# Optimization experiments

Hardware: AMD Instinct MI355X
Metric: run time of the kernel (lower is better)

## Reference

```python
import jax, jax.numpy as jnp
import numpy as np
from jax.scipy.special import erf

ALPHA = 0.84
SSIM_WIN = 11       # monai SSIMLoss default win_size
SIGMA = 1.5         # both kernels use sigma=1.5
K1, K2, DATA_RANGE = 0.01, 0.03, 1.0


def _erf_gauss_1d(sigma=SIGMA, truncated=4.0):
    # monai.networks.layers.gaussian_1d, approx='erf', normalize=False
    tail = int(max(sigma * truncated, 0.5) + 0.5)  # 6 -> 13 taps
    x = jnp.arange(-tail, tail + 1, dtype=jnp.float32)
    t = 0.70710678 / sigma
    out = 0.5 * (erf(t * (x + 0.5)) - erf(t * (x - 0.5)))
    return jnp.clip(out, 0.0)


def _ssim_gauss_1d(win=SSIM_WIN, sigma=SIGMA):
    # monai SSIM gaussian kernel: exp-based, normalized
    d = jnp.arange(-(win - 1) / 2.0, (win + 1) / 2.0, dtype=jnp.float32)
    g = jnp.exp(-(d ** 2) / (2.0 * sigma ** 2))
    return g / g.sum()


def _conv1d(x, k, axis, pad):
    # depthwise 1D conv along spatial axis of NCHW tensor (C=1)
    ks = k.shape[0]
    if axis == 2:
        kern = k.reshape(1, 1, ks, 1)
        p = [(pad, pad), (0, 0)]
    else:
        kern = k.reshape(1, 1, 1, ks)
        p = [(0, 0), (pad, pad)]
    return jax.lax.conv_general_dilated(
        x, kern, window_strides=(1, 1), padding=p,
        dimension_numbers=('NCHW', 'OIHW', 'NCHW'))


def _sep_filter(x, k, pad):
    return _conv1d(_conv1d(x, k, 2, pad), k, 3, pad)


def setup_inputs() -> dict:
    key = jax.random.key(0)
    kx, ky = jax.random.split(key)
    shape = (64, 1, 512, 512)
    x = jax.random.uniform(kx, shape, dtype=jnp.float32)
    y = jax.random.uniform(ky, shape, dtype=jnp.float32)
    return {"x": x, "y": y}


def reference(x, y):
    kw = _ssim_gauss_1d()
    filt = lambda t: _sep_filter(t, kw, 0)
    c1 = (K1 * DATA_RANGE) ** 2
    c2 = (K2 * DATA_RANGE) ** 2
    mx, my = filt(x), filt(y)
    mxx, myy, mxy = filt(x * x), filt(y * y), filt(x * y)
    vx = mxx - mx * mx
    vy = myy - my * my
    cov = mxy - mx * my
    ssim = ((2.0 * mx * my + c1) * (2.0 * cov + c2)) / (
        (mx * mx + my * my + c1) * (vx + vy + c2))
    ssim_loss = 1.0 - jnp.mean(ssim)  # scalar, reduction='mean'

    # --- L1 branch: SAME zero-padded erf-gaussian filtering, no reduction ---
    ke = _erf_gauss_1d()
    pad = (ke.shape[0] - 1) // 2
    l1 = jnp.abs(_sep_filter(y, ke, pad) - _sep_filter(x, ke, pad))  # [N,1,H,W]

    return 100.0 * (ALPHA * ssim_loss + (1.0 - ALPHA) * l1)
```

## Files before the change

### kernel.cpp

```cpp
#include <hip/hip_runtime.h>
#include <cmath>

#define IMG_W 512
#define IMG_H 512
#define NIMG 64
#define OWV 502

struct KTaps {
    float kw[11];
    float ke[13];
};

__global__ __launch_bounds__(256) void ssim_band_kernel(
        const float* __restrict__ x, const float* __restrict__ y,
        double* __restrict__ ssum, KTaps kt) {
    __shared__ __align__(16) float sx[2][272];
    __shared__ __align__(16) float sy[2][272];

    const int img   = blockIdx.z;
    const int band  = blockIdx.y;
    const int strip = blockIdx.x;
    const int tid   = threadIdx.x;
    const int r0    = band * 64;
    const int c0    = strip * 256;

    const float* __restrict__ xi = x + (size_t)img * IMG_H * IMG_W;
    const float* __restrict__ yi = y + (size_t)img * IMG_H * IMG_W;

    float w12[12];
#pragma unroll
    for (int j = 0; j < 12; ++j) w12[j] = 0.f;
    if (tid & 1) {
#pragma unroll
        for (int j = 0; j < 11; ++j) w12[j + 1] = kt.kw[j];
    } else {
#pragma unroll
        for (int j = 0; j < 11; ++j) w12[j] = kt.kw[j];
    }

    float acc[11][5];
#pragma unroll
    for (int i = 0; i < 11; ++i)
#pragma unroll
        for (int q = 0; q < 5; ++q) acc[i][q] = 0.f;
    float tsum = 0.f;

    const int basei = tid & ~1;
    const int outc  = c0 + tid;

    auto ldx = [&](int r, int g) -> float2 {
        float2 v = make_float2(0.f, 0.f);
        if (r < IMG_H && g < IMG_W) v = *(const float2*)(xi + (size_t)r * IMG_W + g);
        return v;
    };
    auto ldy = [&](int r, int g) -> float2 {
        float2 v = make_float2(0.f, 0.f);
        if (r < IMG_H && g < IMG_W) v = *(const float2*)(yi + (size_t)r * IMG_W + g);
        return v;
    };

    if (tid < 133) { float2 v = ldx(r0, c0 + 2 * tid); *(float2*)&sx[0][2 * tid] = v; }
    if (tid >= 123) { const int t3 = tid - 123; float2 v = ldy(r0, c0 + 2 * t3); *(float2*)&sy[0][2 * t3] = v; }
    __syncthreads();

#pragma unroll 1
    for (int chunk = 0; chunk < 7; ++chunk) {
#pragma unroll
        for (int p = 0; p < 11; ++p) {
            const int rr = chunk * 11 + p;
            if (rr <= 73) {
                const int b = rr & 1;
                float2 px = make_float2(0.f, 0.f), py = make_float2(0.f, 0.f);
                const bool pre = (rr < 73);
                if (pre) {
                    if (tid < 133) px = ldx(r0 + rr + 1, c0 + 2 * tid);
                    if (tid >= 123) py = ldy(r0 + rr + 1, c0 + 2 * (tid - 123));
                }
                float xv[12], yv[12];
#pragma unroll
                for (int j = 0; j < 6; ++j) {
                    const float2 a = *(const float2*)&sx[b][basei + 2 * j];
                    const float2 c = *(const float2*)&sy[b][basei + 2 * j];
                    xv[2 * j] = a.x; xv[2 * j + 1] = a.y;
                    yv[2 * j] = c.x; yv[2 * j + 1] = c.y;
                }
                float h0 = 0.f, h1 = 0.f, h2 = 0.f, h3 = 0.f, h4 = 0.f;
#pragma unroll
                for (int j = 0; j < 12; ++j) {
                    const float w = w12[j];
                    const float a = xv[j], bb = yv[j];
                    h0 += w * a;
                    h1 += w * bb;
                    h2 += w * (a * a);
                    h3 += w * (bb * bb);
                    h4 += w * (a * bb);
                }
#pragma unroll
                for (int d = 0; d <= 10; ++d) {
                    const int s = (p + 11 - d) % 11;
                    const float w = kt.kw[d];
                    acc[s][0] += w * h0; acc[s][1] += w * h1; acc[s][2] += w * h2;
                    acc[s][3] += w * h3; acc[s][4] += w * h4;
                }
                {
                    const int sc = (p + 1) % 11;
                    const int ro = rr - 10;
                    if (ro >= 0) {
                        const int o = r0 + ro;
                        if (o < OWV && outc < OWV) {
                            const float mx = acc[sc][0], my = acc[sc][1];
                            const float vx = acc[sc][2] - mx * mx;
                            const float vy = acc[sc][3] - my * my;
                            const float cov = acc[sc][4] - mx * my;
                            const float c1 = 1e-4f, c2 = 9e-4f;
                            tsum += ((2.f * mx * my + c1) * (2.f * cov + c2)) /
                                    ((mx * mx + my * my + c1) * (vx + vy + c2));
                        }
                    }
#pragma unroll
                    for (int q = 0; q < 5; ++q) acc[sc][q] = 0.f;
                }
                if (pre) {
                    const int bn = b ^ 1;
                    if (tid < 133) *(float2*)&sx[bn][2 * tid] = px;
                    if (tid >= 123) *(float2*)&sy[bn][2 * (tid - 123)] = py;
                }
                __syncthreads();
            }
        }
    }

#pragma unroll
    for (int off = 32; off > 0; off >>= 1) tsum += __shfl_down(tsum, off, 64);
    __shared__ float wsum[4];
    const int wid = tid >> 6, lane = tid & 63;
    if (lane == 0) wsum[wid] = tsum;
    __syncthreads();
    if (tid == 0) atomicAdd(ssum, (double)(wsum[0] + wsum[1] + wsum[2] + wsum[3]));
}

__global__ __launch_bounds__(256) void l1_band_kernel(
        const float* __restrict__ x, const float* __restrict__ y,
        const double* __restrict__ ssum, float* __restrict__ out, KTaps kt) {
    __shared__ __align__(16) float sd[2][528];

    const int img  = blockIdx.y;
    const int band = blockIdx.x;
    const int tid  = threadIdx.x;
    const int o0   = band * 32;
    const int rin0 = o0 - 6;

    const float* __restrict__ xi = x + (size_t)img * IMG_H * IMG_W;
    const float* __restrict__ yi = y + (size_t)img * IMG_H * IMG_W;
    float* __restrict__ oi = out + (size_t)img * IMG_H * IMG_W;

    const float base = 100.f * 0.84f * (1.f - (float)(*ssum) * (1.f / 16128256.f));

    float acc[13][2];
#pragma unroll
    for (int i = 0; i < 13; ++i) { acc[i][0] = 0.f; acc[i][1] = 0.f; }

    if (tid < 12) {
        const int idx = (tid < 6) ? tid : (512 + tid);
        sd[0][idx] = 0.f; sd[1][idx] = 0.f;
    }

    auto ldd = [&](int r) -> float2 {
        float2 v = make_float2(0.f, 0.f);
        if (r >= 0 && r < IMG_H) {
            const float2 a = *(const float2*)(xi + (size_t)r * IMG_W + 2 * tid);
            const float2 bb = *(const float2*)(yi + (size_t)r * IMG_W + 2 * tid);
            v = make_float2(bb.x - a.x, bb.y - a.y);
        }
        return v;
    };

    { float2 v = ldd(rin0); *(float2*)&sd[0][6 + 2 * tid] = v; }
    __syncthreads();

#pragma unroll 1
    for (int chunk = 0; chunk < 4; ++chunk) {
#pragma unroll
        for (int p = 0; p < 13; ++p) {
            const int rr = chunk * 13 + p;
            if (rr <= 43) {
                const int b = rr & 1;
                float2 pv = make_float2(0.f, 0.f);
                const bool pre = (rr < 43);
                if (pre) pv = ldd(rin0 + rr + 1);

                float dv[14];
#pragma unroll
                for (int j = 0; j < 7; ++j) {
                    const float2 a = *(const float2*)&sd[b][2 * tid + 2 * j];
                    dv[2 * j] = a.x; dv[2 * j + 1] = a.y;
                }
                float a0 = 0.f, a1 = 0.f;
#pragma unroll
                for (int u = 0; u < 13; ++u) {
                    a0 += kt.ke[u] * dv[u];
                    a1 += kt.ke[u] * dv[u + 1];
                }
#pragma unroll
                for (int dd = 0; dd <= 12; ++dd) {
                    const int s = (p + 13 - dd) % 13;
                    acc[s][0] += kt.ke[dd] * a0;
                    acc[s][1] += kt.ke[dd] * a1;
                }
                {
                    const int sc = (p + 1) % 13;
                    const int ro = rr - 12;
                    if (ro >= 0) {
                        const int o = o0 + ro;
                        *(float2*)&oi[(size_t)o * IMG_W + 2 * tid] =
                            make_float2(base + 16.f * fabsf(acc[sc][0]),
                                        base + 16.f * fabsf(acc[sc][1]));
                    }
                    acc[sc][0] = 0.f; acc[sc][1] = 0.f;
                }
                if (pre) *(float2*)&sd[b ^ 1][6 + 2 * tid] = pv;
                __syncthreads();
            }
        }
    }
}

extern "C" void kernel_launch(void* const* d_in, const int* in_sizes, int n_in,
                              void* d_out, int out_size, void* d_ws, size_t ws_size,
                              hipStream_t stream) {
    const float* x = (const float*)d_in[0];
    const float* y = (const float*)d_in[1];
    float* out = (float*)d_out;
    double* ssum = (double*)d_ws;

    KTaps kt;
    {
        double g[11], s = 0.0;
        for (int i = 0; i < 11; ++i) {
            const double d = (double)i - 5.0;
            g[i] = std::exp(-(d * d) / 4.5);
            s += g[i];
        }
        for (int i = 0; i < 11; ++i) kt.kw[i] = (float)(g[i] / s);
    }
    {
        const double t = 0.70710678 / 1.5;
        for (int i = 0; i < 13; ++i) {
            const double xx = (double)i - 6.0;
            const double v = 0.5 * (std::erf(t * (xx + 0.5)) - std::erf(t * (xx - 0.5)));
            kt.ke[i] = (float)(v < 0.0 ? 0.0 : v);
        }
    }

    hipMemsetAsync(ssum, 0, sizeof(double), stream);

    ssim_band_kernel<<<dim3(2, 8, NIMG), dim3(256), 0, stream>>>(x, y, ssum, kt);
    l1_band_kernel<<<dim3(16, NIMG, 1), dim3(256), 0, stream>>>(x, y, ssum, out, kt);
}
```

Measured before the change: 302.1 us.

## Assign independent tiles per wavefront and drop block-wide barriers

Both kernels now split each block into four wavefronts, and each wavefront owns a narrower column strip with its own private double-buffered shared-memory row. Because only a single wave touches each buffer, the per-row __syncthreads calls are removed. Row staging switches to float4 loads, and the SSIM reduction does one atomic per wave. In exchange, the narrower strips re-read more halo columns, and each wave issues four times as many SSIM atomics.

```diff
diff --git a/kernel.cpp b/kernel.cpp
--- a/kernel.cpp
+++ b/kernel.cpp
@@ -14,23 +14,45 @@
 __global__ __launch_bounds__(256) void ssim_band_kernel(
         const float* __restrict__ x, const float* __restrict__ y,
         double* __restrict__ ssum, KTaps kt) {
-    __shared__ __align__(16) float sx[2][272];
-    __shared__ __align__(16) float sy[2][272];
-
-    const int img   = blockIdx.z;
-    const int band  = blockIdx.y;
-    const int strip = blockIdx.x;
-    const int tid   = threadIdx.x;
-    const int r0    = band * 64;
-    const int c0    = strip * 256;
+    __shared__ __align__(16) float sx[4][2][80];
+    __shared__ __align__(16) float sy[4][2][80];
+
+    const int tid  = threadIdx.x;
+    const int wv   = tid >> 6;
+    const int lane = tid & 63;
+    const int task = blockIdx.x * 4 + wv;
+    const int img   = task >> 6;
+    const int strip = (task >> 3) & 7;
+    const int band  = task & 7;
+    const int r0 = band * 64;
+    const int c0 = strip * 64;
 
     const float* __restrict__ xi = x + (size_t)img * IMG_H * IMG_W;
     const float* __restrict__ yi = y + (size_t)img * IMG_H * IMG_W;
 
+    const bool st_act = (lane < 38);
+    const bool st_x   = (lane < 19);
+    const int  st_k   = st_x ? lane : lane - 19;
+    const int  st_g   = c0 + 4 * st_k;
+    const float* __restrict__ st_arr = st_x ? xi : yi;
+
+    auto ldrow = [&](int r) -> float4 {
+        float4 v = make_float4(0.f, 0.f, 0.f, 0.f);
+        if (st_act && r < IMG_H && st_g < IMG_W)
+            v = *(const float4*)(st_arr + (size_t)r * IMG_W + st_g);
+        return v;
+    };
+    auto strow = [&](int b, float4 v) {
+        if (st_act) {
+            float* dst = st_x ? &sx[wv][b][4 * st_k] : &sy[wv][b][4 * st_k];
+            *(float4*)dst = v;
+        }
+    };
+
     float w12[12];
 #pragma unroll
     for (int j = 0; j < 12; ++j) w12[j] = 0.f;
-    if (tid & 1) {
+    if (lane & 1) {
 #pragma unroll
         for (int j = 0; j < 11; ++j) w12[j + 1] = kt.kw[j];
     } else {
@@ -45,23 +67,10 @@
         for (int q = 0; q < 5; ++q) acc[i][q] = 0.f;
     float tsum = 0.f;
 
-    const int basei = tid & ~1;
-    const int outc  = c0 + tid;
-
-    auto ldx = [&](int r, int g) -> float2 {
-        float2 v = make_float2(0.f, 0.f);
-        if (r < IMG_H && g < IMG_W) v = *(const float2*)(xi + (size_t)r * IMG_W + g);
-        return v;
-    };
-    auto ldy = [&](int r, int g) -> float2 {
-        float2 v = make_float2(0.f, 0.f);
-        if (r < IMG_H && g < IMG_W) v = *(const float2*)(yi + (size_t)r * IMG_W + g);
-        return v;
-    };
-
-    if (tid < 133) { float2 v = ldx(r0, c0 + 2 * tid); *(float2*)&sx[0][2 * tid] = v; }
-    if (tid >= 123) { const int t3 = tid - 123; float2 v = ldy(r0, c0 + 2 * t3); *(float2*)&sy[0][2 * t3] = v; }
-    __syncthreads();
+    const int basei = lane & ~1;
+    const int outc  = c0 + lane;
+
+    strow(0, ldrow(r0));
 
 #pragma unroll 1
     for (int chunk = 0; chunk < 7; ++chunk) {
@@ -70,17 +79,15 @@
             const int rr = chunk * 11 + p;
             if (rr <= 73) {
                 const int b = rr & 1;
-                float2 px = make_float2(0.f, 0.f), py = make_float2(0.f, 0.f);
+                float4 pv = make_float4(0.f, 0.f, 0.f, 0.f);
                 const bool pre = (rr < 73);
-                if (pre) {
-                    if (tid < 133) px = ldx(r0 + rr + 1, c0 + 2 * tid);
-                    if (tid >= 123) py = ldy(r0 + rr + 1, c0 + 2 * (tid - 123));
-                }
+                if (pre) pv = ldrow(r0 + rr + 1);
+
                 float xv[12], yv[12];
 #pragma unroll
                 for (int j = 0; j < 6; ++j) {
-                    const float2 a = *(const float2*)&sx[b][basei + 2 * j];
-                    const float2 c = *(const float2*)&sy[b][basei + 2 * j];
+                    const float2 a = *(const float2*)&sx[wv][b][basei + 2 * j];
+                    const float2 c = *(const float2*)&sy[wv][b][basei + 2 * j];
                     xv[2 * j] = a.x; xv[2 * j + 1] = a.y;
                     yv[2 * j] = c.x; yv[2 * j + 1] = c.y;
                 }
@@ -120,33 +127,30 @@
 #pragma unroll
                     for (int q = 0; q < 5; ++q) acc[sc][q] = 0.f;
                 }
-                if (pre) {
-                    const int bn = b ^ 1;
-                    if (tid < 133) *(float2*)&sx[bn][2 * tid] = px;
-                    if (tid >= 123) *(float2*)&sy[bn][2 * (tid - 123)] = py;
-                }
-                __syncthreads();
+                if (pre) strow(b ^ 1, pv);
             }
         }
     }
 
 #pragma unroll
     for (int off = 32; off > 0; off >>= 1) tsum += __shfl_down(tsum, off, 64);
-    __shared__ float wsum[4];
-    const int wid = tid >> 6, lane = tid & 63;
-    if (lane == 0) wsum[wid] = tsum;
-    __syncthreads();
-    if (tid == 0) atomicAdd(ssum, (double)(wsum[0] + wsum[1] + wsum[2] + wsum[3]));
+    if (lane == 0) atomicAdd(ssum, (double)tsum);
 }
 
 __global__ __launch_bounds__(256) void l1_band_kernel(
         const float* __restrict__ x, const float* __restrict__ y,
         const double* __restrict__ ssum, float* __restrict__ out, KTaps kt) {
-    __shared__ __align__(16) float sd[2][528];
-
-    const int img  = blockIdx.y;
-    const int band = blockIdx.x;
+    __shared__ __align__(16) float sd[4][2][144];
+
     const int tid  = threadIdx.x;
+    const int wv   = tid >> 6;
+    const int lane = tid & 63;
+    const int task = blockIdx.x * 4 + wv;
+    const int img   = task >> 6;
+    const int rem   = task & 63;
+    const int strip = rem >> 4;
+    const int band  = rem & 15;
+    const int C    = strip * 128;
     const int o0   = band * 32;
     const int rin0 = o0 - 6;
 
@@ -156,27 +160,26 @@
 
     const float base = 100.f * 0.84f * (1.f - (float)(*ssum) * (1.f / 16128256.f));
 
+    const bool st_act = (lane < 36);
+    const int  st_g   = C - 8 + 4 * lane;
+    auto ldrow = [&](int r) -> float4 {
+        float4 v = make_float4(0.f, 0.f, 0.f, 0.f);
+        if (st_act && r >= 0 && r < IMG_H && st_g >= 0 && st_g < IMG_W) {
+            const float4 a  = *(const float4*)(xi + (size_t)r * IMG_W + st_g);
+            const float4 bb = *(const float4*)(yi + (size_t)r * IMG_W + st_g);
+            v = make_float4(bb.x - a.x, bb.y - a.y, bb.z - a.z, bb.w - a.w);
+        }
+        return v;
+    };
+    auto strow = [&](int b, float4 v) {
+        if (st_act) *(float4*)&sd[wv][b][4 * lane] = v;
+    };
+
     float acc[13][2];
 #pragma unroll
     for (int i = 0; i < 13; ++i) { acc[i][0] = 0.f; acc[i][1] = 0.f; }
 
-    if (tid < 12) {
-        const int idx = (tid < 6) ? tid : (512 + tid);
-        sd[0][idx] = 0.f; sd[1][idx] = 0.f;
-    }
-
-    auto ldd = [&](int r) -> float2 {
-        float2 v = make_float2(0.f, 0.f);
-        if (r >= 0 && r < IMG_H) {
-            const float2 a = *(const float2*)(xi + (size_t)r * IMG_W + 2 * tid);
-            const float2 bb = *(const float2*)(yi + (size_t)r * IMG_W + 2 * tid);
-            v = make_float2(bb.x - a.x, bb.y - a.y);
-        }
-        return v;
-    };
-
-    { float2 v = ldd(rin0); *(float2*)&sd[0][6 + 2 * tid] = v; }
-    __syncthreads();
+    strow(0, ldrow(rin0));
 
 #pragma unroll 1
     for (int chunk = 0; chunk < 4; ++chunk) {
@@ -185,14 +188,14 @@
             const int rr = chunk * 13 + p;
             if (rr <= 43) {
                 const int b = rr & 1;
-                float2 pv = make_float2(0.f, 0.f);
+                float4 pv = make_float4(0.f, 0.f, 0.f, 0.f);
                 const bool pre = (rr < 43);
-                if (pre) pv = ldd(rin0 + rr + 1);
+                if (pre) pv = ldrow(rin0 + rr + 1);
 
                 float dv[14];
 #pragma unroll
                 for (int j = 0; j < 7; ++j) {
-                    const float2 a = *(const float2*)&sd[b][2 * tid + 2 * j];
+                    const float2 a = *(const float2*)&sd[wv][b][2 * lane + 2 + 2 * j];
                     dv[2 * j] = a.x; dv[2 * j + 1] = a.y;
                 }
                 float a0 = 0.f, a1 = 0.f;
@@ -212,14 +215,13 @@
                     const int ro = rr - 12;
                     if (ro >= 0) {
                         const int o = o0 + ro;
-                        *(float2*)&oi[(size_t)o * IMG_W + 2 * tid] =
+                        *(float2*)&oi[(size_t)o * IMG_W + C + 2 * lane] =
                             make_float2(base + 16.f * fabsf(acc[sc][0]),
                                         base + 16.f * fabsf(acc[sc][1]));
                     }
                     acc[sc][0] = 0.f; acc[sc][1] = 0.f;
                 }
-                if (pre) *(float2*)&sd[b ^ 1][6 + 2 * tid] = pv;
-                __syncthreads();
+                if (pre) strow(b ^ 1, pv);
             }
         }
     }
@@ -254,6 +256,6 @@
 
     hipMemsetAsync(ssum, 0, sizeof(double), stream);
 
-    ssim_band_kernel<<<dim3(2, 8, NIMG), dim3(256), 0, stream>>>(x, y, ssum, kt);
-    l1_band_kernel<<<dim3(16, NIMG, 1), dim3(256), 0, stream>>>(x, y, ssum, out, kt);
+    ssim_band_kernel<<<dim3(1024), dim3(256), 0, stream>>>(x, y, ssum, kt);
+    l1_band_kernel<<<dim3(1024), dim3(256), 0, stream>>>(x, y, ssum, out, kt);
 }
```

New measurement: 303.4 us. Within noise of the previous version (+0.4%).
